# Kernel tuning notes

Hardware: AMD Instinct MI355X
Metric: run time of the kernel (lower is better)

The kernel has to match this reference:

```python
import jax, jax.numpy as jnp
import numpy as np

SLOPE = 5.0                # surrogate gradient slope (SurrogateGradient default)
REFRACTORY_PERIOD = 2.0    # config.refractory_period
ADAPT_DECAY = 0.9          # threshold_adapt EMA decay
ADAPT_INC = 0.1


@jax.custom_vjp
def spike_fn(membrane, threshold):
    # Heaviside spike with surrogate gradient (fast sigmoid), matching SurrogateGradient
    return (membrane >= threshold).astype(membrane.dtype)

def _spike_fwd(membrane, threshold):
    return spike_fn(membrane, threshold), (membrane, threshold)

def _spike_bwd(res, g):
    membrane, threshold = res
    s = jax.nn.sigmoid(SLOPE * (membrane - threshold))
    grad_m = g * SLOPE * s * (1.0 - s)
    # torch returns None (zero) grad for threshold through the spike op itself
    return grad_m, jnp.zeros_like(threshold)

spike_fn.defvjp(_spike_fwd, _spike_bwd)


def setup_inputs() -> dict:
    key = jax.random.key(0)
    kx, = jax.random.split(key, 1)
    B, S, D = 16, 2048, 1024
    x = jax.random.normal(kx, (B, S, D), dtype=jnp.float32)
    beta_mem = jnp.asarray(0.9, dtype=jnp.float32)                      # membrane_decay
    beta_syn = jnp.exp(jnp.asarray(-1.0 / 5.0, dtype=jnp.float32))      # exp(-1/tau_syn)
    threshold_adapt_p = jnp.full((1,), 0.1, dtype=jnp.float32)          # nn.Parameter ones(1)*0.1
    threshold_scale = jnp.ones((D,), dtype=jnp.float32)
    learnable_threshold = jnp.ones((D,), dtype=jnp.float32)             # threshold=1.0
    return {
        "x": x,
        "beta_mem": beta_mem,
        "beta_syn": beta_syn,
        "threshold_adapt_p": threshold_adapt_p,
        "threshold_scale": threshold_scale,
        "learnable_threshold": learnable_threshold,
    }


def _lif(x, beta_mem, beta_syn, threshold_adapt_p, threshold_scale, learnable_threshold):
    B, S, D = x.shape
    z = jnp.zeros((B, D), dtype=x.dtype)
    init = (z, z, z, z)  # membrane, synaptic, threshold_adapt, refractory

    def step(carry, xt):  # xt: (B, D)
        membrane, synaptic, th_adapt, refractory = carry
        synaptic = beta_syn * synaptic + xt
        non_refractory = (refractory <= 0).astype(x.dtype)
        membrane = beta_mem * membrane + synaptic * non_refractory
        cur_th = learnable_threshold + threshold_adapt_p * th_adapt * threshold_scale
        spikes = spike_fn(membrane, cur_th)
        membrane = membrane - spikes * cur_th  # reset_mode='subtract'
        th_adapt = ADAPT_DECAY * th_adapt + ADAPT_INC * spikes
        refractory = jnp.where(
            spikes > 0.5,
            jnp.full_like(spikes, REFRACTORY_PERIOD),
            jnp.clip(refractory - 1.0, 0.0),
        )
        return (membrane, synaptic, th_adapt, refractory), spikes

    carry, spikes = jax.lax.scan(step, init, jnp.swapaxes(x, 0, 1))  # scan over seq
    spike_train = jnp.swapaxes(spikes, 0, 1)  # (B, S, D)
    return spike_train, carry


def reference(x, beta_mem, beta_syn, threshold_adapt_p, threshold_scale, learnable_threshold):
    spike_train, (membrane, synaptic, th_adapt, refractory) = _lif(
        x, beta_mem, beta_syn, threshold_adapt_p, threshold_scale, learnable_threshold
    )
    return spike_train, membrane, synaptic, th_adapt, refractory
```

## Files before the change

kernel.cpp:

```cpp
#include <hip/hip_runtime.h>
#include <stdint.h>


#define SB 16
#define SS 2048
#define SD 1024
#define TILE 64
#define NT (SS / TILE)

typedef const __attribute__((address_space(1))) void* gas_ptr;
typedef __attribute__((address_space(3))) void* las_ptr;

__global__ __launch_bounds__(64, 1) void lif_kernel(
    const float* __restrict__ x,
    const float* __restrict__ beta_mem_p,
    const float* __restrict__ beta_syn_p,
    const float* __restrict__ adapt_p,
    const float* __restrict__ scale_p,
    const float* __restrict__ lth_p,
    float* __restrict__ out)
{
#pragma clang fp contract(off)
    __shared__ __attribute__((aligned(16))) float lds[3][TILE][64];

    const int bk   = blockIdx.x;
    const int b    = bk >> 4;
    const int d0   = (bk & 15) << 6;
    const int lane = threadIdx.x;
    const int d    = d0 + lane;

    const float beta_mem = beta_mem_p[0];
    const float beta_syn = beta_syn_p[0];
    const float p        = adapt_p[0];
    const float scale    = scale_p[d];
    const float lth      = lth_p[d];

    const float* xb   = x   + ((size_t)b * SS) * SD + d0;
    float*       outb = out + ((size_t)b * SS) * SD + d0;

    const int srow = lane >> 4;
    const int scol = (lane & 15) << 2;
    const float* src_base = xb + (size_t)srow * SD + scol;

    auto issue_tile = [&](int k, int buf) {
        const float* s0 = src_base + (size_t)(k * TILE) * SD;
        float* dst = &lds[buf][0][0];
        #pragma unroll
        for (int r = 0; r < 16; ++r) {
            __builtin_amdgcn_global_load_lds(
                (gas_ptr)(s0 + (size_t)(r * 4) * SD),
                (las_ptr)(dst + r * 4 * 64),
                16, 0, 0);
        }
    };

    float mem = 0.f, syn = 0.f, tha = 0.f, refr = 0.f;
    int sidx = lane;

    auto step = [&](float xt) {
        syn = __builtin_fmaf(beta_syn, syn, xt);
        const bool  nref    = (refr <= 0.f);
        const float syn_eff = nref ? syn : 0.f;
        mem = __builtin_fmaf(beta_mem, mem, syn_eff);
        const float q      = p * tha;
        const float cur_th = __builtin_fmaf(q, scale, lth);
        const bool  fired  = (mem >= cur_th);
        const float spike  = fired ? 1.f : 0.f;
        mem = mem - (fired ? cur_th : 0.f);
        tha = __builtin_fmaf(0.9f, tha, fired ? 0.1f : 0.f);
        const float rnext = fmaxf(refr - 1.f, 0.f);
        refr = fired ? 2.0f : rnext;
        outb[sidx] = spike;
        sidx += SD;
    };

    issue_tile(0, 0);
    issue_tile(1, 1);
    asm volatile("s_waitcnt vmcnt(16)" ::: "memory");

    int cbuf = 0;
    for (int k = 0; k < NT; ++k) {
        asm volatile("s_waitcnt vmcnt(63)" ::: "memory");
        __builtin_amdgcn_sched_barrier(0);

        if (k + 2 < NT) {
            const int nbuf = (cbuf + 2 >= 3) ? cbuf - 1 : cbuf + 2;
            issue_tile(k + 2, nbuf);
        }

        float xa[16], xbv[16], xc[16], xd[16];
        #pragma unroll
        for (int i = 0; i < 16; ++i) xa[i]  = lds[cbuf][i][lane];
        #pragma unroll
        for (int i = 0; i < 16; ++i) xbv[i] = lds[cbuf][16 + i][lane];
        #pragma unroll
        for (int i = 0; i < 16; ++i) xc[i]  = lds[cbuf][32 + i][lane];
        #pragma unroll
        for (int i = 0; i < 16; ++i) xd[i]  = lds[cbuf][48 + i][lane];

        #pragma unroll
        for (int i = 0; i < 16; ++i) step(xa[i]);
        #pragma unroll
        for (int i = 0; i < 16; ++i) step(xbv[i]);
        #pragma unroll
        for (int i = 0; i < 16; ++i) step(xc[i]);
        #pragma unroll
        for (int i = 0; i < 16; ++i) step(xd[i]);

        cbuf = (cbuf == 2) ? 0 : cbuf + 1;
    }

    const size_t base = (size_t)SB * SS * SD;
    const size_t off  = (size_t)b * SD + d;
    out[base + 0 * (size_t)SB * SD + off] = mem;
    out[base + 1 * (size_t)SB * SD + off] = syn;
    out[base + 2 * (size_t)SB * SD + off] = tha;
    out[base + 3 * (size_t)SB * SD + off] = refr;
}

extern "C" void kernel_launch(void* const* d_in, const int* in_sizes, int n_in,
                              void* d_out, int out_size, void* d_ws, size_t ws_size,
                              hipStream_t stream) {
    const float* x        = (const float*)d_in[0];
    const float* beta_mem = (const float*)d_in[1];
    const float* beta_syn = (const float*)d_in[2];
    const float* adapt_p  = (const float*)d_in[3];
    const float* scale    = (const float*)d_in[4];
    const float* lth      = (const float*)d_in[5];
    float* out = (float*)d_out;

    lif_kernel<<<256, 64, 0, stream>>>(x, beta_mem, beta_syn, adapt_p, scale, lth, out);
}
```

Measured before the change: 90.66 us.

## Split LIF kernel into compute wave and producer wave for loads and stores

The block grows from one wave to two. One wave runs the serial LIF recurrence and writes spikes into a padded LDS staging buffer. The second wave issues the async global-to-LDS loads for x and writes the spike tiles out to global memory, and the two waves hand off each tile with a barrier. The refractory counter is also swapped for two boolean fired flags. The aim is to take the per-step global stores and load issue off the critical recurrence path, at the cost of a per-tile __syncthreads and a correctness dependence on the barrier ordering. The vmcnt waits were removed, so load completion now relies on the barrier.

```diff
diff --git a/kernel.cpp b/kernel.cpp
--- a/kernel.cpp
+++ b/kernel.cpp
@@ -11,7 +11,7 @@
 typedef const __attribute__((address_space(1))) void* gas_ptr;
 typedef __attribute__((address_space(3))) void* las_ptr;
 
-__global__ __launch_bounds__(64, 1) void lif_kernel(
+__global__ __launch_bounds__(128, 1) void lif_kernel(
     const float* __restrict__ x,
     const float* __restrict__ beta_mem_p,
     const float* __restrict__ beta_syn_p,
@@ -21,101 +21,125 @@
     float* __restrict__ out)
 {
 #pragma clang fp contract(off)
-    __shared__ __attribute__((aligned(16))) float lds[3][TILE][64];
+    __shared__ __attribute__((aligned(16))) float xbuf[3][TILE][64];
+    __shared__ float sbuf[2][64][TILE + 1];
 
-    const int bk   = blockIdx.x;
-    const int b    = bk >> 4;
-    const int d0   = (bk & 15) << 6;
-    const int lane = threadIdx.x;
-    const int d    = d0 + lane;
+    const int bk = blockIdx.x;
+    const int b  = bk >> 4;
+    const int d0 = (bk & 15) << 6;
 
-    const float beta_mem = beta_mem_p[0];
-    const float beta_syn = beta_syn_p[0];
-    const float p        = adapt_p[0];
-    const float scale    = scale_p[d];
-    const float lth      = lth_p[d];
+    if (threadIdx.x < 64) {
+        const int lane = threadIdx.x;
+        const int d    = d0 + lane;
 
-    const float* xb   = x   + ((size_t)b * SS) * SD + d0;
-    float*       outb = out + ((size_t)b * SS) * SD + d0;
+        const float beta_mem = beta_mem_p[0];
+        const float beta_syn = beta_syn_p[0];
+        const float p        = adapt_p[0];
+        const float scale    = scale_p[d];
+        const float lth      = lth_p[d];
 
-    const int srow = lane >> 4;
-    const int scol = (lane & 15) << 2;
-    const float* src_base = xb + (size_t)srow * SD + scol;
+        float mem = 0.f, syn = 0.f, tha = 0.f;
+        bool  nref = true;
+        bool  f1 = false, f2 = false;
 
-    auto issue_tile = [&](int k, int buf) {
-        const float* s0 = src_base + (size_t)(k * TILE) * SD;
-        float* dst = &lds[buf][0][0];
-        #pragma unroll
-        for (int r = 0; r < 16; ++r) {
-            __builtin_amdgcn_global_load_lds(
-                (gas_ptr)(s0 + (size_t)(r * 4) * SD),
-                (las_ptr)(dst + r * 4 * 64),
-                16, 0, 0);
-        }
-    };
+        __syncthreads();
 
-    float mem = 0.f, syn = 0.f, tha = 0.f, refr = 0.f;
-    int sidx = lane;
+        int cbuf = 0;
+        for (int k = 0; k < NT; ++k) {
+            const int sb = k & 1;
 
-    auto step = [&](float xt) {
-        syn = __builtin_fmaf(beta_syn, syn, xt);
-        const bool  nref    = (refr <= 0.f);
-        const float syn_eff = nref ? syn : 0.f;
-        mem = __builtin_fmaf(beta_mem, mem, syn_eff);
-        const float q      = p * tha;
-        const float cur_th = __builtin_fmaf(q, scale, lth);
-        const bool  fired  = (mem >= cur_th);
-        const float spike  = fired ? 1.f : 0.f;
-        mem = mem - (fired ? cur_th : 0.f);
-        tha = __builtin_fmaf(0.9f, tha, fired ? 0.1f : 0.f);
-        const float rnext = fmaxf(refr - 1.f, 0.f);
-        refr = fired ? 2.0f : rnext;
-        outb[sidx] = spike;
-        sidx += SD;
-    };
+            float xa[16], xbv[16], xc[16], xd[16];
+            #pragma unroll
+            for (int i = 0; i < 16; ++i) xa[i]  = xbuf[cbuf][i][lane];
+            #pragma unroll
+            for (int i = 0; i < 16; ++i) xbv[i] = xbuf[cbuf][16 + i][lane];
+            #pragma unroll
+            for (int i = 0; i < 16; ++i) xc[i]  = xbuf[cbuf][32 + i][lane];
+            #pragma unroll
+            for (int i = 0; i < 16; ++i) xd[i]  = xbuf[cbuf][48 + i][lane];
 
-    issue_tile(0, 0);
-    issue_tile(1, 1);
-    asm volatile("s_waitcnt vmcnt(16)" ::: "memory");
+            auto step = [&](float xt, int ti) {
+                syn = __builtin_fmaf(beta_syn, syn, xt);
+                const float syn_eff = nref ? syn : 0.f;
+                mem = __builtin_fmaf(beta_mem, mem, syn_eff);
+                const float q      = p * tha;
+                const float cur_th = __builtin_fmaf(q, scale, lth);
+                const bool  fired  = (mem >= cur_th);
+                const float spike  = fired ? 1.f : 0.f;
+                mem = mem - (fired ? cur_th : 0.f);
+                tha = __builtin_fmaf(0.9f, tha, fired ? 0.1f : 0.f);
+                nref = !(fired || f1);
+                f2 = f1; f1 = fired;
+                sbuf[sb][lane][ti] = spike;
+            };
 
-    int cbuf = 0;
-    for (int k = 0; k < NT; ++k) {
-        asm volatile("s_waitcnt vmcnt(63)" ::: "memory");
-        __builtin_amdgcn_sched_barrier(0);
+            #pragma unroll
+            for (int i = 0; i < 16; ++i) step(xa[i], i);
+            #pragma unroll
+            for (int i = 0; i < 16; ++i) step(xbv[i], 16 + i);
+            #pragma unroll
+            for (int i = 0; i < 16; ++i) step(xc[i], 32 + i);
+            #pragma unroll
+            for (int i = 0; i < 16; ++i) step(xd[i], 48 + i);
 
-        if (k + 2 < NT) {
-            const int nbuf = (cbuf + 2 >= 3) ? cbuf - 1 : cbuf + 2;
-            issue_tile(k + 2, nbuf);
+            __syncthreads();
+            cbuf = (cbuf == 2) ? 0 : cbuf + 1;
         }
 
-        float xa[16], xbv[16], xc[16], xd[16];
-        #pragma unroll
-        for (int i = 0; i < 16; ++i) xa[i]  = lds[cbuf][i][lane];
-        #pragma unroll
-        for (int i = 0; i < 16; ++i) xbv[i] = lds[cbuf][16 + i][lane];
-        #pragma unroll
-        for (int i = 0; i < 16; ++i) xc[i]  = lds[cbuf][32 + i][lane];
-        #pragma unroll
-        for (int i = 0; i < 16; ++i) xd[i]  = lds[cbuf][48 + i][lane];
+        const float refr = f1 ? 2.0f : (f2 ? 1.0f : 0.0f);
+        const size_t base = (size_t)SB * SS * SD;
+        const size_t off  = (size_t)b * SD + d;
+        out[base + 0 * (size_t)SB * SD + off] = mem;
+        out[base + 1 * (size_t)SB * SD + off] = syn;
+        out[base + 2 * (size_t)SB * SD + off] = tha;
+        out[base + 3 * (size_t)SB * SD + off] = refr;
+    } else {
+        const int hl = threadIdx.x - 64;
 
-        #pragma unroll
-        for (int i = 0; i < 16; ++i) step(xa[i]);
-        #pragma unroll
-        for (int i = 0; i < 16; ++i) step(xbv[i]);
-        #pragma unroll
-        for (int i = 0; i < 16; ++i) step(xc[i]);
-        #pragma unroll
-        for (int i = 0; i < 16; ++i) step(xd[i]);
+        const float* xb   = x   + ((size_t)b * SS) * SD + d0;
+        float*       outb = out + ((size_t)b * SS) * SD + d0;
 
-        cbuf = (cbuf == 2) ? 0 : cbuf + 1;
+        const int srow = hl >> 4;
+        const int scol = (hl & 15) << 2;
+        const float* src_base = xb + (size_t)srow * SD + scol;
+
+        auto issue_tile = [&](int k, int buf) {
+            const float* s0 = src_base + (size_t)(k * TILE) * SD;
+            float* dst = &xbuf[buf][0][0];
+            #pragma unroll
+            for (int r = 0; r < 16; ++r) {
+                __builtin_amdgcn_global_load_lds(
+                    (gas_ptr)(s0 + (size_t)(r * 4) * SD),
+                    (las_ptr)(dst + r * 4 * 64),
+                    16, 0, 0);
+            }
+        };
+
+        auto store_tile = [&](int tk) {
+            const int sb = tk & 1;
+            int idx = tk * TILE * SD + hl;
+            #pragma unroll 8
+            for (int t = 0; t < TILE; ++t) {
+                outb[idx] = sbuf[sb][hl][t];
+                idx += SD;
+            }
+        };
+
+        issue_tile(0, 0);
+        issue_tile(1, 1);
+        __syncthreads();
+
+        int nbuf = 2;
+        for (int k = 0; k < NT; ++k) {
+            if (k + 2 < NT) {
+                issue_tile(k + 2, nbuf);
+                nbuf = (nbuf == 2) ? 0 : nbuf + 1;
+            }
+            if (k >= 1) store_tile(k - 1);
+            __syncthreads();
+        }
+        store_tile(NT - 1);
     }
-
-    const size_t base = (size_t)SB * SS * SD;
-    const size_t off  = (size_t)b * SD + d;
-    out[base + 0 * (size_t)SB * SD + off] = mem;
-    out[base + 1 * (size_t)SB * SD + off] = syn;
-    out[base + 2 * (size_t)SB * SD + off] = tha;
-    out[base + 3 * (size_t)SB * SD + off] = refr;
 }
 
 extern "C" void kernel_launch(void* const* d_in, const int* in_sizes, int n_in,
@@ -129,5 +153,5 @@
     const float* lth      = (const float*)d_in[5];
     float* out = (float*)d_out;
 
-    lif_kernel<<<256, 64, 0, stream>>>(x, beta_mem, beta_syn, adapt_p, scale, lth, out);
+    lif_kernel<<<256, 128, 0, stream>>>(x, beta_mem, beta_syn, adapt_p, scale, lth, out);
 }
```

Measured after the change: 79.49 us. -12.3%, faster.
